# Kernel optimization log

Measured on AMD Instinct MI355X. Metric: run time of the kernel, lower is better.

The kernel has to match this reference:

```python
import jax, jax.numpy as jnp
import numpy as np

B, D, S, K = 4096, 256, 32, 32
TEMP = 1.0

def _unit(x):
    return x / jnp.linalg.norm(x, axis=-1, keepdims=True)

def setup_inputs() -> dict:
    key = jax.random.key(0)
    k1, k2, k3, k4 = jax.random.split(key, 4)
    return {
        "embeddings": _unit(jax.random.normal(k1, (B, D), dtype=jnp.float32)),
        "similar_malicious_embeddings": _unit(jax.random.normal(k2, (B, S, D), dtype=jnp.float32)),
        "diverse_malicious_embeddings": _unit(jax.random.normal(k3, (B, K, D), dtype=jnp.float32)),
        "labels": jax.random.randint(k4, (B,), 0, 2, dtype=jnp.int64),
    }

def reference(embeddings, similar_malicious_embeddings, diverse_malicious_embeddings, labels):
    b = embeddings.shape[0]
    # all pairwise sims zi . zj / T  -> [B, B]
    sims = jnp.matmul(embeddings, embeddings.T) / TEMP
    # sims of zi vs its own similar/diverse sets -> [B, S], [B, K]
    sim_s = jnp.einsum('bd,bsd->bs', embeddings, similar_malicious_embeddings) / TEMP
    sim_d = jnp.einsum('bd,bkd->bk', embeddings, diverse_malicious_embeddings) / TEMP
    not_self = ~jnp.eye(b, dtype=bool)
    # denominator over c_xi = (all embeddings except i) + similar_i + diverse_i
    denom = (jnp.exp(sims) * not_self).sum(-1) + jnp.exp(sim_s).sum(-1) + jnp.exp(sim_d).sum(-1)
    mal = labels == 1
    # d_xi = malicious others (b1_xi) + similar_i + diverse_i
    b1_mask = mal[None, :] & not_self  # [B, B]
    sum_num = (sims * b1_mask).sum(-1) + sim_s.sum(-1) + sim_d.sum(-1)
    cnt = b1_mask.sum(-1) + sim_s.shape[1] + sim_d.shape[1]  # |d_xi| per i (>0 since S,K>0)
    # per zp: -log(exp(s_zp)/denom); averaged over d_xi
    per_i = -sum_num / cnt.astype(sims.dtype) + jnp.log(denom)
    loss = jnp.where(mal, per_i, 0.0).sum() / b
    return loss
```

## Files before the change

kernel.cpp:

```cpp
#include <hip/hip_runtime.h>
#include <stdint.h>

#define BTOT 4096
#define DD   256
#define SS   32
#define KKN  32

typedef unsigned short u16;
using f32x4  = __attribute__((ext_vector_type(4))) float;
using bf16x8 = __attribute__((ext_vector_type(8))) short;

__device__ __forceinline__ u16 f2bf(float f) {
    uint32_t u = __builtin_bit_cast(uint32_t, f);
    u = (u + 0x7FFFu + ((u >> 16) & 1u)) >> 16;
    return (u16)u;
}
__device__ __forceinline__ float bf2f(u16 h) {
    uint32_t u = ((uint32_t)h) << 16;
    return __builtin_bit_cast(float, u);
}

__global__ __launch_bounds__(256) void cast_kernel(const float* __restrict__ E,
                                                   u16* __restrict__ ebf) {
    int idx = blockIdx.x * 256 + threadIdx.x;
    const float4* p = reinterpret_cast<const float4*>(E) + (size_t)idx * 2;
    float4 a = p[0], b = p[1];
    uint4 o;
    o.x = (uint32_t)f2bf(a.x) | ((uint32_t)f2bf(a.y) << 16);
    o.y = (uint32_t)f2bf(a.z) | ((uint32_t)f2bf(a.w) << 16);
    o.z = (uint32_t)f2bf(b.x) | ((uint32_t)f2bf(b.y) << 16);
    o.w = (uint32_t)f2bf(b.z) | ((uint32_t)f2bf(b.w) << 16);
    reinterpret_cast<uint4*>(ebf)[idx] = o;
}

__global__ __launch_bounds__(256) void gemm_kernel(
    const u16* __restrict__ ebf, const int* __restrict__ labels,
    float* __restrict__ gden, float* __restrict__ gnum)
{
    __shared__ u16 As[128 * 32];
    __shared__ u16 Bs[128 * 32];
    __shared__ float rbuf[2][2][128];
    __shared__ float cbuf[2][2][128];

    int bid = blockIdx.x;
    int R = (int)((65.0f - sqrtf(4225.0f - 8.0f * (float)bid)) * 0.5f);
    while (R > 0 && R * (65 - R) / 2 > bid) --R;
    while ((R + 1) * (64 - R) / 2 <= bid) ++R;
    int C = R + (bid - R * (65 - R) / 2);

    int brow = R * 128, bcol = C * 128;
    int t = threadIdx.x, w = t >> 6, lane = t & 63;
    int wr = w >> 1, wc = w & 1;
    int r16 = lane & 15, hi = lane >> 4;
    int kq = hi * 8;

    f32x4 acc[4][4] = {};

    for (int kt = 0; kt < DD / 32; ++kt) {
        int k0 = kt * 32;
        #pragma unroll
        for (int it = 0; it < 2; ++it) {
            int c   = t + 256 * it;
            int row = c >> 2;
            int col = (c & 3) * 8;
            const u16* ga = &ebf[(size_t)(brow + row) * DD + k0 + col];
            const u16* gb = &ebf[(size_t)(bcol + row) * DD + k0 + col];
            __builtin_amdgcn_global_load_lds(
                (const __attribute__((address_space(1))) unsigned int*)ga,
                (__attribute__((address_space(3))) unsigned int*)&As[c * 8], 16, 0, 0);
            __builtin_amdgcn_global_load_lds(
                (const __attribute__((address_space(1))) unsigned int*)gb,
                (__attribute__((address_space(3))) unsigned int*)&Bs[c * 8], 16, 0, 0);
        }
        __syncthreads();

        bf16x8 af[4], bfr[4];
        #pragma unroll
        for (int m = 0; m < 4; ++m)
            af[m] = *(const bf16x8*)&As[(wr * 64 + m * 16 + r16) * 32 + kq];
        #pragma unroll
        for (int n = 0; n < 4; ++n)
            bfr[n] = *(const bf16x8*)&Bs[(wc * 64 + n * 16 + r16) * 32 + kq];
        #pragma unroll
        for (int m = 0; m < 4; ++m)
            #pragma unroll
            for (int n = 0; n < 4; ++n)
                acc[m][n] = __builtin_amdgcn_mfma_f32_16x16x32_bf16(af[m], bfr[n], acc[m][n], 0, 0, 0);
        __syncthreads();
    }

    bool offdiag = (C != R);

    float malf[4];
    #pragma unroll
    for (int n = 0; n < 4; ++n)
        malf[n] = (float)labels[bcol + wc * 64 + n * 16 + r16];
    float malr[16];
    #pragma unroll
    for (int m = 0; m < 4; ++m)
        #pragma unroll
        for (int r = 0; r < 4; ++r)
            malr[m * 4 + r] = (float)labels[brow + wr * 64 + m * 16 + hi * 4 + r];

    float cd[4] = {0.f, 0.f, 0.f, 0.f}, cn[4] = {0.f, 0.f, 0.f, 0.f};

    #pragma unroll
    for (int m = 0; m < 4; ++m) {
        #pragma unroll
        for (int r = 0; r < 4; ++r) {
            float pe = 0.f, pn = 0.f;
            #pragma unroll
            for (int n = 0; n < 4; ++n) {
                float v  = acc[m][n][r];
                float ex = __expf(v);
                pe += ex;
                pn += malf[n] * v;
                cd[n] += ex;
                cn[n] += malr[m * 4 + r] * v;
            }
            #pragma unroll
            for (int s = 1; s < 16; s <<= 1) {
                pe += __shfl_xor(pe, s, 64);
                pn += __shfl_xor(pn, s, 64);
            }
            if (r16 == 0) {
                int rl = wr * 64 + m * 16 + hi * 4 + r;
                rbuf[0][wc][rl] = pe;
                rbuf[1][wc][rl] = pn;
            }
        }
    }

    if (offdiag) {
        #pragma unroll
        for (int n = 0; n < 4; ++n) {
            cd[n] += __shfl_xor(cd[n], 16, 64);
            cd[n] += __shfl_xor(cd[n], 32, 64);
            cn[n] += __shfl_xor(cn[n], 16, 64);
            cn[n] += __shfl_xor(cn[n], 32, 64);
            if (lane < 16) {
                int cl = wc * 64 + n * 16 + lane;
                cbuf[0][wr][cl] = cd[n];
                cbuf[1][wr][cl] = cn[n];
            }
        }
    }
    __syncthreads();

    if (t < 128) {
        int i = brow + t;
        gden[(size_t)i * 32 + C] = rbuf[0][0][t] + rbuf[0][1][t];
        gnum[(size_t)i * 32 + C] = rbuf[1][0][t] + rbuf[1][1][t];
    } else if (offdiag) {
        int tt = t - 128;
        int j = bcol + tt;
        gden[(size_t)j * 32 + R] = cbuf[0][0][tt] + cbuf[0][1][tt];
        gnum[(size_t)j * 32 + R] = cbuf[1][0][tt] + cbuf[1][1][tt];
    }
}

__global__ __launch_bounds__(256) void simdiv_kernel(
    const float* __restrict__ E, const float* __restrict__ Sim, const float* __restrict__ Div,
    const int* __restrict__ labels, float* __restrict__ sdden, float* __restrict__ sdnum)
{
    extern __shared__ float lds[];
    int i = blockIdx.x;
    int t = threadIdx.x, w = t >> 6, lane = t & 63;
    int g = lane >> 4, sub = lane & 15;

    const float4* E4 = reinterpret_cast<const float4*>(E + (size_t)i * DD);
    float4 e0 = E4[0 * 16 + sub], e1 = E4[1 * 16 + sub];
    float4 e2 = E4[2 * 16 + sub], e3 = E4[3 * 16 + sub];

    #pragma unroll
    for (int vt = 0; vt < 16; ++vt) {
        int v = w * 16 + vt;
        const float* src = (v < SS) ? (Sim + ((size_t)i * SS + v) * DD)
                                    : (Div + ((size_t)i * KKN + (v - SS)) * DD);
        __builtin_amdgcn_global_load_lds(
            (const __attribute__((address_space(1))) unsigned int*)(src + lane * 4),
            (__attribute__((address_space(3))) unsigned int*)(lds + (size_t)v * DD), 16, 0, 0);
    }

    float accs = 0.f, acce = 0.f;

#define SD_STEP(VT, CNT)                                                          \
    {                                                                             \
        asm volatile("s_waitcnt vmcnt(" #CNT ")" ::: "memory");                   \
        int v = w * 16 + (VT) * 4 + g;                                            \
        const float4* row = reinterpret_cast<const float4*>(lds + (size_t)v * DD);\
        float4 s0 = row[0 * 16 + sub], s1 = row[1 * 16 + sub];                    \
        float4 s2 = row[2 * 16 + sub], s3 = row[3 * 16 + sub];                    \
        float d = e0.x * s0.x + e0.y * s0.y + e0.z * s0.z + e0.w * s0.w           \
                + e1.x * s1.x + e1.y * s1.y + e1.z * s1.z + e1.w * s1.w           \
                + e2.x * s2.x + e2.y * s2.y + e2.z * s2.z + e2.w * s2.w           \
                + e3.x * s3.x + e3.y * s3.y + e3.z * s3.z + e3.w * s3.w;          \
        d += __shfl_xor(d, 1, 64);                                                \
        d += __shfl_xor(d, 2, 64);                                                \
        d += __shfl_xor(d, 4, 64);                                                \
        d += __shfl_xor(d, 8, 64);                                                \
        accs += d;                                                                \
        acce += __expf(d);                                                        \
    }

    SD_STEP(0, 12)
    SD_STEP(1, 8)
    SD_STEP(2, 4)
    SD_STEP(3, 0)
#undef SD_STEP

    accs += __shfl_xor(accs, 16, 64);
    accs += __shfl_xor(accs, 32, 64);
    acce += __shfl_xor(acce, 16, 64);
    acce += __shfl_xor(acce, 32, 64);

    float sd = 0.f;
    {
        float c;
        c = bf2f(f2bf(e0.x)); sd += c * c;  c = bf2f(f2bf(e0.y)); sd += c * c;
        c = bf2f(f2bf(e0.z)); sd += c * c;  c = bf2f(f2bf(e0.w)); sd += c * c;
        c = bf2f(f2bf(e1.x)); sd += c * c;  c = bf2f(f2bf(e1.y)); sd += c * c;
        c = bf2f(f2bf(e1.z)); sd += c * c;  c = bf2f(f2bf(e1.w)); sd += c * c;
        c = bf2f(f2bf(e2.x)); sd += c * c;  c = bf2f(f2bf(e2.y)); sd += c * c;
        c = bf2f(f2bf(e2.z)); sd += c * c;  c = bf2f(f2bf(e2.w)); sd += c * c;
        c = bf2f(f2bf(e3.x)); sd += c * c;  c = bf2f(f2bf(e3.y)); sd += c * c;
        c = bf2f(f2bf(e3.z)); sd += c * c;  c = bf2f(f2bf(e3.w)); sd += c * c;
    }
    sd += __shfl_xor(sd, 1, 64);
    sd += __shfl_xor(sd, 2, 64);
    sd += __shfl_xor(sd, 4, 64);
    sd += __shfl_xor(sd, 8, 64);

    if (lane == 0) {
        float addn = accs, addd = acce;
        if (w == 0) {
            addd -= __expf(sd);
            addn -= (float)labels[i] * sd;
        }
        atomicAdd(&sdnum[i], addn);
        atomicAdd(&sdden[i], addd);
    }
}

__global__ __launch_bounds__(128) void reduce1_kernel(
    const int* __restrict__ labels, const float* __restrict__ gden,
    const float* __restrict__ gnum, const float* __restrict__ sdden,
    const float* __restrict__ sdnum, float* __restrict__ part)
{
    __shared__ float sA[128], sB[128];
    __shared__ int   sC[128];
    int p = blockIdx.x, t = threadIdx.x;
    int i = p * 128 + t;

    const float4* dr = reinterpret_cast<const float4*>(gden + (size_t)i * 32);
    const float4* nr = reinterpret_cast<const float4*>(gnum + (size_t)i * 32);
    float den = sdden[i], num = sdnum[i];
    #pragma unroll
    for (int c = 0; c < 8; ++c) {
        float4 a = dr[c]; den += a.x + a.y + a.z + a.w;
        float4 b = nr[c]; num += b.x + b.y + b.z + b.w;
    }
    int lab = labels[i];
    sA[t] = lab ? __logf(den) : 0.f;
    sB[t] = lab ? num : 0.f;
    sC[t] = lab;
    __syncthreads();
    for (int s = 64; s > 0; s >>= 1) {
        if (t < s) { sA[t] += sA[t + s]; sB[t] += sB[t + s]; sC[t] += sC[t + s]; }
        __syncthreads();
    }
    if (t == 0) {
        part[p]      = sA[0];
        part[32 + p] = sB[0];
        part[64 + p] = (float)sC[0];
    }
}

__global__ __launch_bounds__(64) void final_kernel(const float* __restrict__ part,
                                                   float* __restrict__ out)
{
    int lane = threadIdx.x;
    float lg = (lane < 32) ? part[lane]      : 0.f;
    float nm = (lane < 32) ? part[32 + lane] : 0.f;
    float ml = (lane < 32) ? part[64 + lane] : 0.f;
    #pragma unroll
    for (int s = 1; s < 64; s <<= 1) {
        lg += __shfl_xor(lg, s, 64);
        nm += __shfl_xor(nm, s, 64);
        ml += __shfl_xor(ml, s, 64);
    }
    if (lane == 0) {
        float cnt = ml - 1.f + (float)(SS + KKN);
        out[0] = (lg - nm / cnt) / (float)BTOT;
    }
}

extern "C" void kernel_launch(void* const* d_in, const int* in_sizes, int n_in,
                              void* d_out, int out_size, void* d_ws, size_t ws_size,
                              hipStream_t stream) {
    const float* E   = (const float*)d_in[0];
    const float* Sim = (const float*)d_in[1];
    const float* Div = (const float*)d_in[2];
    const int* labels = (const int*)d_in[3];
    float* out = (float*)d_out;

    char* ws = (char*)d_ws;
    u16*   ebf   = (u16*)ws;                              ws += (size_t)BTOT * DD * sizeof(u16);
    float* gden  = (float*)ws;                            ws += (size_t)BTOT * 32 * sizeof(float);
    float* gnum  = (float*)ws;                            ws += (size_t)BTOT * 32 * sizeof(float);
    float* sdden = (float*)ws;                            ws += BTOT * sizeof(float);
    float* sdnum = (float*)ws;                            ws += BTOT * sizeof(float);
    float* part  = (float*)ws;

    hipMemsetAsync(sdden, 0, 2 * BTOT * sizeof(float), stream);
    cast_kernel<<<BTOT * DD / 8 / 256, 256, 0, stream>>>(E, ebf);
    gemm_kernel<<<528, 256, 0, stream>>>(ebf, labels, gden, gnum);
    simdiv_kernel<<<BTOT, 256, 64 * 1024, stream>>>(E, Sim, Div, labels, sdden, sdnum);
    reduce1_kernel<<<32, 128, 0, stream>>>(labels, gden, gnum, sdden, sdnum, part);
    final_kernel<<<1, 64, 0, stream>>>(part, out);
}
```

Before: 78.55 us.

## Merge GEMM and sim/div kernels into one interleaved launch, drop memset and atomics

```diff
diff --git a/kernel.cpp b/kernel.cpp
--- a/kernel.cpp
+++ b/kernel.cpp
@@ -5,6 +5,8 @@
 #define DD   256
 #define SS   32
 #define KKN  32
+#define NGEMM 528
+#define NBLK  (BTOT + NGEMM)
 
 typedef unsigned short u16;
 using f32x4  = __attribute__((ext_vector_type(4))) float;
@@ -33,156 +35,163 @@
     reinterpret_cast<uint4*>(ebf)[idx] = o;
 }
 
-__global__ __launch_bounds__(256) void gemm_kernel(
+__global__ __launch_bounds__(256) void fat_kernel(
+    const float* __restrict__ E, const float* __restrict__ Sim, const float* __restrict__ Div,
     const u16* __restrict__ ebf, const int* __restrict__ labels,
-    float* __restrict__ gden, float* __restrict__ gnum)
+    float* __restrict__ gden, float* __restrict__ gnum,
+    float* __restrict__ sdden, float* __restrict__ sdnum)
 {
-    __shared__ u16 As[128 * 32];
-    __shared__ u16 Bs[128 * 32];
-    __shared__ float rbuf[2][2][128];
-    __shared__ float cbuf[2][2][128];
-
-    int bid = blockIdx.x;
-    int R = (int)((65.0f - sqrtf(4225.0f - 8.0f * (float)bid)) * 0.5f);
-    while (R > 0 && R * (65 - R) / 2 > bid) --R;
-    while ((R + 1) * (64 - R) / 2 <= bid) ++R;
-    int C = R + (bid - R * (65 - R) / 2);
-
-    int brow = R * 128, bcol = C * 128;
-    int t = threadIdx.x, w = t >> 6, lane = t & 63;
-    int wr = w >> 1, wc = w & 1;
-    int r16 = lane & 15, hi = lane >> 4;
-    int kq = hi * 8;
-
-    f32x4 acc[4][4] = {};
-
-    for (int kt = 0; kt < DD / 32; ++kt) {
-        int k0 = kt * 32;
+    extern __shared__ char dyn[];
+    int bid  = blockIdx.x;
+    int t    = threadIdx.x;
+    int w    = t >> 6;
+    int lane = t & 63;
+
+    bool is_gemm = (bid < NGEMM * 8) && ((bid & 7) == 7);
+
+    if (is_gemm) {
+        u16*   As   = (u16*)dyn;
+        u16*   Bs   = (u16*)(dyn + 8192);
+        float* rbuf = (float*)(dyn + 16384);
+        float* cbuf = (float*)(dyn + 16384 + 2048);
+
+        int g = bid >> 3;
+        int R = (int)((65.0f - sqrtf(4225.0f - 8.0f * (float)g)) * 0.5f);
+        while (R > 0 && R * (65 - R) / 2 > g) --R;
+        while ((R + 1) * (64 - R) / 2 <= g) ++R;
+        int C = R + (g - R * (65 - R) / 2);
+
+        int brow = R * 128, bcol = C * 128;
+        int wr = w >> 1, wc = w & 1;
+        int r16 = lane & 15, hi = lane >> 4;
+        int kq = hi * 8;
+
+        f32x4 acc[4][4] = {};
+
+        for (int kt = 0; kt < DD / 32; ++kt) {
+            int k0 = kt * 32;
+            #pragma unroll
+            for (int it = 0; it < 2; ++it) {
+                int c   = t + 256 * it;
+                int row = c >> 2;
+                int col = (c & 3) * 8;
+                const u16* ga = &ebf[(size_t)(brow + row) * DD + k0 + col];
+                const u16* gb = &ebf[(size_t)(bcol + row) * DD + k0 + col];
+                __builtin_amdgcn_global_load_lds(
+                    (const __attribute__((address_space(1))) unsigned int*)ga,
+                    (__attribute__((address_space(3))) unsigned int*)&As[c * 8], 16, 0, 0);
+                __builtin_amdgcn_global_load_lds(
+                    (const __attribute__((address_space(1))) unsigned int*)gb,
+                    (__attribute__((address_space(3))) unsigned int*)&Bs[c * 8], 16, 0, 0);
+            }
+            __syncthreads();
+
+            bf16x8 af[4], bfr[4];
+            #pragma unroll
+            for (int m = 0; m < 4; ++m)
+                af[m] = *(const bf16x8*)&As[(wr * 64 + m * 16 + r16) * 32 + kq];
+            #pragma unroll
+            for (int n = 0; n < 4; ++n)
+                bfr[n] = *(const bf16x8*)&Bs[(wc * 64 + n * 16 + r16) * 32 + kq];
+            #pragma unroll
+            for (int m = 0; m < 4; ++m)
+                #pragma unroll
+                for (int n = 0; n < 4; ++n)
+                    acc[m][n] = __builtin_amdgcn_mfma_f32_16x16x32_bf16(af[m], bfr[n], acc[m][n], 0, 0, 0);
+            __syncthreads();
+        }
+
+        bool offdiag = (C != R);
+
+        float malf[4];
         #pragma unroll
-        for (int it = 0; it < 2; ++it) {
-            int c   = t + 256 * it;
-            int row = c >> 2;
-            int col = (c & 3) * 8;
-            const u16* ga = &ebf[(size_t)(brow + row) * DD + k0 + col];
-            const u16* gb = &ebf[(size_t)(bcol + row) * DD + k0 + col];
-            __builtin_amdgcn_global_load_lds(
-                (const __attribute__((address_space(1))) unsigned int*)ga,
-                (__attribute__((address_space(3))) unsigned int*)&As[c * 8], 16, 0, 0);
-            __builtin_amdgcn_global_load_lds(
-                (const __attribute__((address_space(1))) unsigned int*)gb,
-                (__attribute__((address_space(3))) unsigned int*)&Bs[c * 8], 16, 0, 0);
-        }
-        __syncthreads();
-
-        bf16x8 af[4], bfr[4];
+        for (int n = 0; n < 4; ++n)
+            malf[n] = (float)labels[bcol + wc * 64 + n * 16 + r16];
+        float malr[16];
         #pragma unroll
         for (int m = 0; m < 4; ++m)
-            af[m] = *(const bf16x8*)&As[(wr * 64 + m * 16 + r16) * 32 + kq];
+            #pragma unroll
+            for (int r = 0; r < 4; ++r)
+                malr[m * 4 + r] = (float)labels[brow + wr * 64 + m * 16 + hi * 4 + r];
+
+        float cd[4] = {0.f, 0.f, 0.f, 0.f}, cn[4] = {0.f, 0.f, 0.f, 0.f};
+
         #pragma unroll
-        for (int n = 0; n < 4; ++n)
-            bfr[n] = *(const bf16x8*)&Bs[(wc * 64 + n * 16 + r16) * 32 + kq];
+        for (int m = 0; m < 4; ++m) {
+            #pragma unroll
+            for (int r = 0; r < 4; ++r) {
+                float pe = 0.f, pn = 0.f;
+                #pragma unroll
+                for (int n = 0; n < 4; ++n) {
+                    float v  = acc[m][n][r];
+                    float ex = __expf(v);
+                    pe += ex;
+                    pn += malf[n] * v;
+                    cd[n] += ex;
+                    cn[n] += malr[m * 4 + r] * v;
+                }
+                #pragma unroll
+                for (int s = 1; s < 16; s <<= 1) {
+                    pe += __shfl_xor(pe, s, 64);
+                    pn += __shfl_xor(pn, s, 64);
+                }
+                if (r16 == 0) {
+                    int rl = wr * 64 + m * 16 + hi * 4 + r;
+                    rbuf[0 * 256 + wc * 128 + rl] = pe;
+                    rbuf[1 * 256 + wc * 128 + rl] = pn;
+                }
+            }
+        }
+
+        if (offdiag) {
+            #pragma unroll
+            for (int n = 0; n < 4; ++n) {
+                cd[n] += __shfl_xor(cd[n], 16, 64);
+                cd[n] += __shfl_xor(cd[n], 32, 64);
+                cn[n] += __shfl_xor(cn[n], 16, 64);
+                cn[n] += __shfl_xor(cn[n], 32, 64);
+                if (lane < 16) {
+                    int cl = wc * 64 + n * 16 + lane;
+                    cbuf[0 * 256 + wr * 128 + cl] = cd[n];
+                    cbuf[1 * 256 + wr * 128 + cl] = cn[n];
+                }
+            }
+        }
+        __syncthreads();
+
+        if (t < 128) {
+            int i = brow + t;
+            gden[(size_t)i * 32 + C] = rbuf[0 * 256 + 0 + t] + rbuf[0 * 256 + 128 + t];
+            gnum[(size_t)i * 32 + C] = rbuf[1 * 256 + 0 + t] + rbuf[1 * 256 + 128 + t];
+        } else if (offdiag) {
+            int tt = t - 128;
+            int j = bcol + tt;
+            gden[(size_t)j * 32 + R] = cbuf[0 * 256 + 0 + tt] + cbuf[0 * 256 + 128 + tt];
+            gnum[(size_t)j * 32 + R] = cbuf[1 * 256 + 0 + tt] + cbuf[1 * 256 + 128 + tt];
+        }
+    } else {
+        float* lds  = (float*)dyn;
+        float* sbuf = (float*)(dyn + 64 * 1024);
+
+        int i = (bid < NGEMM * 8) ? bid - (bid >> 3) : bid - NGEMM;
+        int g = lane >> 4, sub = lane & 15;
+
+        const float4* E4 = reinterpret_cast<const float4*>(E + (size_t)i * DD);
+        float4 e0 = E4[0 * 16 + sub], e1 = E4[1 * 16 + sub];
+        float4 e2 = E4[2 * 16 + sub], e3 = E4[3 * 16 + sub];
+        asm volatile("" ::: "memory");
+
         #pragma unroll
-        for (int m = 0; m < 4; ++m)
-            #pragma unroll
-            for (int n = 0; n < 4; ++n)
-                acc[m][n] = __builtin_amdgcn_mfma_f32_16x16x32_bf16(af[m], bfr[n], acc[m][n], 0, 0, 0);
-        __syncthreads();
-    }
-
-    bool offdiag = (C != R);
-
-    float malf[4];
-    #pragma unroll
-    for (int n = 0; n < 4; ++n)
-        malf[n] = (float)labels[bcol + wc * 64 + n * 16 + r16];
-    float malr[16];
-    #pragma unroll
-    for (int m = 0; m < 4; ++m)
-        #pragma unroll
-        for (int r = 0; r < 4; ++r)
-            malr[m * 4 + r] = (float)labels[brow + wr * 64 + m * 16 + hi * 4 + r];
-
-    float cd[4] = {0.f, 0.f, 0.f, 0.f}, cn[4] = {0.f, 0.f, 0.f, 0.f};
-
-    #pragma unroll
-    for (int m = 0; m < 4; ++m) {
-        #pragma unroll
-        for (int r = 0; r < 4; ++r) {
-            float pe = 0.f, pn = 0.f;
-            #pragma unroll
-            for (int n = 0; n < 4; ++n) {
-                float v  = acc[m][n][r];
-                float ex = __expf(v);
-                pe += ex;
-                pn += malf[n] * v;
-                cd[n] += ex;
-                cn[n] += malr[m * 4 + r] * v;
-            }
-            #pragma unroll
-            for (int s = 1; s < 16; s <<= 1) {
-                pe += __shfl_xor(pe, s, 64);
-                pn += __shfl_xor(pn, s, 64);
-            }
-            if (r16 == 0) {
-                int rl = wr * 64 + m * 16 + hi * 4 + r;
-                rbuf[0][wc][rl] = pe;
-                rbuf[1][wc][rl] = pn;
-            }
-        }
-    }
-
-    if (offdiag) {
-        #pragma unroll
-        for (int n = 0; n < 4; ++n) {
-            cd[n] += __shfl_xor(cd[n], 16, 64);
-            cd[n] += __shfl_xor(cd[n], 32, 64);
-            cn[n] += __shfl_xor(cn[n], 16, 64);
-            cn[n] += __shfl_xor(cn[n], 32, 64);
-            if (lane < 16) {
-                int cl = wc * 64 + n * 16 + lane;
-                cbuf[0][wr][cl] = cd[n];
-                cbuf[1][wr][cl] = cn[n];
-            }
-        }
-    }
-    __syncthreads();
-
-    if (t < 128) {
-        int i = brow + t;
-        gden[(size_t)i * 32 + C] = rbuf[0][0][t] + rbuf[0][1][t];
-        gnum[(size_t)i * 32 + C] = rbuf[1][0][t] + rbuf[1][1][t];
-    } else if (offdiag) {
-        int tt = t - 128;
-        int j = bcol + tt;
-        gden[(size_t)j * 32 + R] = cbuf[0][0][tt] + cbuf[0][1][tt];
-        gnum[(size_t)j * 32 + R] = cbuf[1][0][tt] + cbuf[1][1][tt];
-    }
-}
-
-__global__ __launch_bounds__(256) void simdiv_kernel(
-    const float* __restrict__ E, const float* __restrict__ Sim, const float* __restrict__ Div,
-    const int* __restrict__ labels, float* __restrict__ sdden, float* __restrict__ sdnum)
-{
-    extern __shared__ float lds[];
-    int i = blockIdx.x;
-    int t = threadIdx.x, w = t >> 6, lane = t & 63;
-    int g = lane >> 4, sub = lane & 15;
-
-    const float4* E4 = reinterpret_cast<const float4*>(E + (size_t)i * DD);
-    float4 e0 = E4[0 * 16 + sub], e1 = E4[1 * 16 + sub];
-    float4 e2 = E4[2 * 16 + sub], e3 = E4[3 * 16 + sub];
-
-    #pragma unroll
-    for (int vt = 0; vt < 16; ++vt) {
-        int v = w * 16 + vt;
-        const float* src = (v < SS) ? (Sim + ((size_t)i * SS + v) * DD)
-                                    : (Div + ((size_t)i * KKN + (v - SS)) * DD);
-        __builtin_amdgcn_global_load_lds(
-            (const __attribute__((address_space(1))) unsigned int*)(src + lane * 4),
-            (__attribute__((address_space(3))) unsigned int*)(lds + (size_t)v * DD), 16, 0, 0);
-    }
-
-    float accs = 0.f, acce = 0.f;
+        for (int vt = 0; vt < 16; ++vt) {
+            int v = w * 16 + vt;
+            const float* src = (v < SS) ? (Sim + ((size_t)i * SS + v) * DD)
+                                        : (Div + ((size_t)i * KKN + (v - SS)) * DD);
+            __builtin_amdgcn_global_load_lds(
+                (const __attribute__((address_space(1))) unsigned int*)(src + lane * 4),
+                (__attribute__((address_space(3))) unsigned int*)(lds + (size_t)v * DD), 16, 0, 0);
+        }
+
+        float accs = 0.f, acce = 0.f;
 
 #define SD_STEP(VT, CNT)                                                          \
     {                                                                             \
@@ -203,42 +212,49 @@
         acce += __expf(d);                                                        \
     }
 
-    SD_STEP(0, 12)
-    SD_STEP(1, 8)
-    SD_STEP(2, 4)
-    SD_STEP(3, 0)
+        SD_STEP(0, 12)
+        SD_STEP(1, 8)
+        SD_STEP(2, 4)
+        SD_STEP(3, 0)
 #undef SD_STEP
 
-    accs += __shfl_xor(accs, 16, 64);
-    accs += __shfl_xor(accs, 32, 64);
-    acce += __shfl_xor(acce, 16, 64);
-    acce += __shfl_xor(acce, 32, 64);
-
-    float sd = 0.f;
-    {
-        float c;
-        c = bf2f(f2bf(e0.x)); sd += c * c;  c = bf2f(f2bf(e0.y)); sd += c * c;
-        c = bf2f(f2bf(e0.z)); sd += c * c;  c = bf2f(f2bf(e0.w)); sd += c * c;
-        c = bf2f(f2bf(e1.x)); sd += c * c;  c = bf2f(f2bf(e1.y)); sd += c * c;
-        c = bf2f(f2bf(e1.z)); sd += c * c;  c = bf2f(f2bf(e1.w)); sd += c * c;
-        c = bf2f(f2bf(e2.x)); sd += c * c;  c = bf2f(f2bf(e2.y)); sd += c * c;
-        c = bf2f(f2bf(e2.z)); sd += c * c;  c = bf2f(f2bf(e2.w)); sd += c * c;
-        c = bf2f(f2bf(e3.x)); sd += c * c;  c = bf2f(f2bf(e3.y)); sd += c * c;
-        c = bf2f(f2bf(e3.z)); sd += c * c;  c = bf2f(f2bf(e3.w)); sd += c * c;
-    }
-    sd += __shfl_xor(sd, 1, 64);
-    sd += __shfl_xor(sd, 2, 64);
-    sd += __shfl_xor(sd, 4, 64);
-    sd += __shfl_xor(sd, 8, 64);
-
-    if (lane == 0) {
-        float addn = accs, addd = acce;
+        accs += __shfl_xor(accs, 16, 64);
+        accs += __shfl_xor(accs, 32, 64);
+        acce += __shfl_xor(acce, 16, 64);
+        acce += __shfl_xor(acce, 32, 64);
+
+        float sd = 0.f;
         if (w == 0) {
-            addd -= __expf(sd);
-            addn -= (float)labels[i] * sd;
-        }
-        atomicAdd(&sdnum[i], addn);
-        atomicAdd(&sdden[i], addd);
+            float c;
+            c = bf2f(f2bf(e0.x)); sd += c * c;  c = bf2f(f2bf(e0.y)); sd += c * c;
+            c = bf2f(f2bf(e0.z)); sd += c * c;  c = bf2f(f2bf(e0.w)); sd += c * c;
+            c = bf2f(f2bf(e1.x)); sd += c * c;  c = bf2f(f2bf(e1.y)); sd += c * c;
+            c = bf2f(f2bf(e1.z)); sd += c * c;  c = bf2f(f2bf(e1.w)); sd += c * c;
+            c = bf2f(f2bf(e2.x)); sd += c * c;  c = bf2f(f2bf(e2.y)); sd += c * c;
+            c = bf2f(f2bf(e2.z)); sd += c * c;  c = bf2f(f2bf(e2.w)); sd += c * c;
+            c = bf2f(f2bf(e3.x)); sd += c * c;  c = bf2f(f2bf(e3.y)); sd += c * c;
+            c = bf2f(f2bf(e3.z)); sd += c * c;  c = bf2f(f2bf(e3.w)); sd += c * c;
+            sd += __shfl_xor(sd, 1, 64);
+            sd += __shfl_xor(sd, 2, 64);
+            sd += __shfl_xor(sd, 4, 64);
+            sd += __shfl_xor(sd, 8, 64);
+        }
+
+        __syncthreads();
+        if (lane == 0) {
+            float addn = accs, addd = acce;
+            if (w == 0) {
+                addd -= __expf(sd);
+                addn -= (float)labels[i] * sd;
+            }
+            sbuf[w * 2]     = addn;
+            sbuf[w * 2 + 1] = addd;
+        }
+        __syncthreads();
+        if (t == 0) {
+            sdnum[i] = sbuf[0] + sbuf[2] + sbuf[4] + sbuf[6];
+            sdden[i] = sbuf[1] + sbuf[3] + sbuf[5] + sbuf[7];
+        }
     }
 }
 
@@ -305,17 +321,16 @@
     float* out = (float*)d_out;
 
     char* ws = (char*)d_ws;
-    u16*   ebf   = (u16*)ws;                              ws += (size_t)BTOT * DD * sizeof(u16);
-    float* gden  = (float*)ws;                            ws += (size_t)BTOT * 32 * sizeof(float);
-    float* gnum  = (float*)ws;                            ws += (size_t)BTOT * 32 * sizeof(float);
-    float* sdden = (float*)ws;                            ws += BTOT * sizeof(float);
-    float* sdnum = (float*)ws;                            ws += BTOT * sizeof(float);
+    u16*   ebf   = (u16*)ws;   ws += (size_t)BTOT * DD * sizeof(u16);
+    float* gden  = (float*)ws; ws += (size_t)BTOT * 32 * sizeof(float);
+    float* gnum  = (float*)ws; ws += (size_t)BTOT * 32 * sizeof(float);
+    float* sdden = (float*)ws; ws += BTOT * sizeof(float);
+    float* sdnum = (float*)ws; ws += BTOT * sizeof(float);
     float* part  = (float*)ws;
 
-    hipMemsetAsync(sdden, 0, 2 * BTOT * sizeof(float), stream);
     cast_kernel<<<BTOT * DD / 8 / 256, 256, 0, stream>>>(E, ebf);
-    gemm_kernel<<<528, 256, 0, stream>>>(ebf, labels, gden, gnum);
-    simdiv_kernel<<<BTOT, 256, 64 * 1024, stream>>>(E, Sim, Div, labels, sdden, sdnum);
+    fat_kernel<<<NBLK, 256, 64 * 1024 + 64, stream>>>(E, Sim, Div, ebf, labels,
+                                                      gden, gnum, sdden, sdnum);
     reduce1_kernel<<<32, 128, 0, stream>>>(labels, gden, gnum, sdden, sdnum, part);
     final_kernel<<<1, 64, 0, stream>>>(part, out);
 }
```

Result: slower. 105.0 us (+33.7%).

## Pipeline simdiv over 8 rows per block and drop atomics and memset

Applied to the files above, without the earlier changes.

```diff
diff --git a/kernel.cpp b/kernel.cpp
--- a/kernel.cpp
+++ b/kernel.cpp
@@ -5,6 +5,9 @@
 #define DD   256
 #define SS   32
 #define KKN  32
+#define NGEMM 528
+#define NROWB 8
+#define SDBLK (BTOT / NROWB)
 
 typedef unsigned short u16;
 using f32x4  = __attribute__((ext_vector_type(4))) float;
@@ -161,91 +164,134 @@
 
 __global__ __launch_bounds__(256) void simdiv_kernel(
     const float* __restrict__ E, const float* __restrict__ Sim, const float* __restrict__ Div,
-    const int* __restrict__ labels, float* __restrict__ sdden, float* __restrict__ sdnum)
+    float* __restrict__ sdpart)
 {
-    extern __shared__ float lds[];
-    int i = blockIdx.x;
+    extern __shared__ char dyn[];
+    float* stg = (float*)dyn;
+    float* eld = (float*)(dyn + 65536);
+    float* scr = (float*)(dyn + 65536 + 8192);
+
+    int b = blockIdx.x;
     int t = threadIdx.x, w = t >> 6, lane = t & 63;
     int g = lane >> 4, sub = lane & 15;
-
-    const float4* E4 = reinterpret_cast<const float4*>(E + (size_t)i * DD);
-    float4 e0 = E4[0 * 16 + sub], e1 = E4[1 * 16 + sub];
-    float4 e2 = E4[2 * 16 + sub], e3 = E4[3 * 16 + sub];
-
-    #pragma unroll
-    for (int vt = 0; vt < 16; ++vt) {
-        int v = w * 16 + vt;
-        const float* src = (v < SS) ? (Sim + ((size_t)i * SS + v) * DD)
-                                    : (Div + ((size_t)i * KKN + (v - SS)) * DD);
-        __builtin_amdgcn_global_load_lds(
-            (const __attribute__((address_space(1))) unsigned int*)(src + lane * 4),
-            (__attribute__((address_space(3))) unsigned int*)(lds + (size_t)v * DD), 16, 0, 0);
-    }
-
-    float accs = 0.f, acce = 0.f;
-
-#define SD_STEP(VT, CNT)                                                          \
-    {                                                                             \
-        asm volatile("s_waitcnt vmcnt(" #CNT ")" ::: "memory");                   \
-        int v = w * 16 + (VT) * 4 + g;                                            \
-        const float4* row = reinterpret_cast<const float4*>(lds + (size_t)v * DD);\
-        float4 s0 = row[0 * 16 + sub], s1 = row[1 * 16 + sub];                    \
-        float4 s2 = row[2 * 16 + sub], s3 = row[3 * 16 + sub];                    \
-        float d = e0.x * s0.x + e0.y * s0.y + e0.z * s0.z + e0.w * s0.w           \
-                + e1.x * s1.x + e1.y * s1.y + e1.z * s1.z + e1.w * s1.w           \
-                + e2.x * s2.x + e2.y * s2.y + e2.z * s2.z + e2.w * s2.w           \
-                + e3.x * s3.x + e3.y * s3.y + e3.z * s3.z + e3.w * s3.w;          \
-        d += __shfl_xor(d, 1, 64);                                                \
-        d += __shfl_xor(d, 2, 64);                                                \
-        d += __shfl_xor(d, 4, 64);                                                \
-        d += __shfl_xor(d, 8, 64);                                                \
-        accs += d;                                                                \
-        acce += __expf(d);                                                        \
-    }
-
-    SD_STEP(0, 12)
-    SD_STEP(1, 8)
-    SD_STEP(2, 4)
-    SD_STEP(3, 0)
-#undef SD_STEP
-
-    accs += __shfl_xor(accs, 16, 64);
-    accs += __shfl_xor(accs, 32, 64);
-    acce += __shfl_xor(acce, 16, 64);
-    acce += __shfl_xor(acce, 32, 64);
-
-    float sd = 0.f;
-    {
-        float c;
-        c = bf2f(f2bf(e0.x)); sd += c * c;  c = bf2f(f2bf(e0.y)); sd += c * c;
-        c = bf2f(f2bf(e0.z)); sd += c * c;  c = bf2f(f2bf(e0.w)); sd += c * c;
-        c = bf2f(f2bf(e1.x)); sd += c * c;  c = bf2f(f2bf(e1.y)); sd += c * c;
-        c = bf2f(f2bf(e1.z)); sd += c * c;  c = bf2f(f2bf(e1.w)); sd += c * c;
-        c = bf2f(f2bf(e2.x)); sd += c * c;  c = bf2f(f2bf(e2.y)); sd += c * c;
-        c = bf2f(f2bf(e2.z)); sd += c * c;  c = bf2f(f2bf(e2.w)); sd += c * c;
-        c = bf2f(f2bf(e3.x)); sd += c * c;  c = bf2f(f2bf(e3.y)); sd += c * c;
-        c = bf2f(f2bf(e3.z)); sd += c * c;  c = bf2f(f2bf(e3.w)); sd += c * c;
-    }
-    sd += __shfl_xor(sd, 1, 64);
-    sd += __shfl_xor(sd, 2, 64);
-    sd += __shfl_xor(sd, 4, 64);
-    sd += __shfl_xor(sd, 8, 64);
-
-    if (lane == 0) {
-        float addn = accs, addd = acce;
-        if (w == 0) {
-            addd -= __expf(sd);
-            addn -= (float)labels[i] * sd;
-        }
-        atomicAdd(&sdnum[i], addn);
-        atomicAdd(&sdden[i], addd);
-    }
+    int i0 = b * NROWB;
+
+    float* wstg = stg + w * 16 * 256;
+    float* weld = eld + w * 2 * 256;
+
+#define STAGE_E(I, P)                                                                        \
+    __builtin_amdgcn_global_load_lds(                                                        \
+        (const __attribute__((address_space(1))) unsigned int*)(E + (size_t)(I) * DD + lane * 4), \
+        (__attribute__((address_space(3))) unsigned int*)(weld + (P) * 256), 16, 0, 0)
+
+#define STAGE_V(I, Q)                                                                        \
+    {                                                                                        \
+        int v_ = w * 16 + (Q);                                                               \
+        const float* s_ = (v_ < SS) ? (Sim + ((size_t)(I) * SS + v_) * DD)                   \
+                                    : (Div + ((size_t)(I) * KKN + (v_ - SS)) * DD);          \
+        __builtin_amdgcn_global_load_lds(                                                    \
+            (const __attribute__((address_space(1))) unsigned int*)(s_ + lane * 4),          \
+            (__attribute__((address_space(3))) unsigned int*)(wstg + (Q) * 256), 16, 0, 0);  \
+    }
+
+#define COMP(CC)                                                                             \
+    {                                                                                        \
+        const float4* row_ = (const float4*)(wstg + ((CC) * 4 + g) * 256);                   \
+        float4 s0 = row_[0 * 16 + sub], s1 = row_[1 * 16 + sub];                             \
+        float4 s2 = row_[2 * 16 + sub], s3 = row_[3 * 16 + sub];                             \
+        float d = e0.x * s0.x + e0.y * s0.y + e0.z * s0.z + e0.w * s0.w                      \
+                + e1.x * s1.x + e1.y * s1.y + e1.z * s1.z + e1.w * s1.w                      \
+                + e2.x * s2.x + e2.y * s2.y + e2.z * s2.z + e2.w * s2.w                      \
+                + e3.x * s3.x + e3.y * s3.y + e3.z * s3.z + e3.w * s3.w;                     \
+        d += __shfl_xor(d, 1, 64);                                                           \
+        d += __shfl_xor(d, 2, 64);                                                           \
+        d += __shfl_xor(d, 4, 64);                                                           \
+        d += __shfl_xor(d, 8, 64);                                                           \
+        accs += d;                                                                           \
+        acce += __expf(d);                                                                   \
+    }
+
+    STAGE_E(i0, 0);
+    #pragma unroll
+    for (int q = 0; q < 16; ++q) STAGE_V(i0, q);
+
+    #pragma unroll 1
+    for (int r = 0; r < NROWB; ++r) {
+        int i = i0 + r;
+        int p = r & 1;
+        bool more = (r < NROWB - 1);
+
+        float accs = 0.f, acce = 0.f;
+        float4 e0, e1, e2, e3;
+
+        asm volatile("s_waitcnt vmcnt(12)" ::: "memory");
+        {
+            const float4* ep = (const float4*)(weld + p * 256);
+            e0 = ep[0 * 16 + sub]; e1 = ep[1 * 16 + sub];
+            e2 = ep[2 * 16 + sub]; e3 = ep[3 * 16 + sub];
+        }
+        COMP(0)
+        if (more) {
+            STAGE_E(i + 1, p ^ 1);
+            STAGE_V(i + 1, 0) STAGE_V(i + 1, 1) STAGE_V(i + 1, 2) STAGE_V(i + 1, 3)
+        }
+
+        if (more) { asm volatile("s_waitcnt vmcnt(13)" ::: "memory"); }
+        else      { asm volatile("s_waitcnt vmcnt(8)"  ::: "memory"); }
+        COMP(1)
+        if (more) { STAGE_V(i + 1, 4) STAGE_V(i + 1, 5) STAGE_V(i + 1, 6) STAGE_V(i + 1, 7) }
+
+        if (more) { asm volatile("s_waitcnt vmcnt(13)" ::: "memory"); }
+        else      { asm volatile("s_waitcnt vmcnt(4)"  ::: "memory"); }
+        COMP(2)
+        if (more) { STAGE_V(i + 1, 8) STAGE_V(i + 1, 9) STAGE_V(i + 1, 10) STAGE_V(i + 1, 11) }
+
+        if (more) { asm volatile("s_waitcnt vmcnt(13)" ::: "memory"); }
+        else      { asm volatile("s_waitcnt vmcnt(0)"  ::: "memory"); }
+        COMP(3)
+        if (more) { STAGE_V(i + 1, 12) STAGE_V(i + 1, 13) STAGE_V(i + 1, 14) STAGE_V(i + 1, 15) }
+
+        accs += __shfl_xor(accs, 16, 64);
+        accs += __shfl_xor(accs, 32, 64);
+        acce += __shfl_xor(acce, 16, 64);
+        acce += __shfl_xor(acce, 32, 64);
+
+        float sd = 0.f;
+        {
+            float c;
+            c = bf2f(f2bf(e0.x)); sd += c * c;  c = bf2f(f2bf(e0.y)); sd += c * c;
+            c = bf2f(f2bf(e0.z)); sd += c * c;  c = bf2f(f2bf(e0.w)); sd += c * c;
+            c = bf2f(f2bf(e1.x)); sd += c * c;  c = bf2f(f2bf(e1.y)); sd += c * c;
+            c = bf2f(f2bf(e1.z)); sd += c * c;  c = bf2f(f2bf(e1.w)); sd += c * c;
+            c = bf2f(f2bf(e2.x)); sd += c * c;  c = bf2f(f2bf(e2.y)); sd += c * c;
+            c = bf2f(f2bf(e2.z)); sd += c * c;  c = bf2f(f2bf(e2.w)); sd += c * c;
+            c = bf2f(f2bf(e3.x)); sd += c * c;  c = bf2f(f2bf(e3.y)); sd += c * c;
+            c = bf2f(f2bf(e3.z)); sd += c * c;  c = bf2f(f2bf(e3.w)); sd += c * c;
+        }
+        sd += __shfl_xor(sd, 1, 64);
+        sd += __shfl_xor(sd, 2, 64);
+        sd += __shfl_xor(sd, 4, 64);
+        sd += __shfl_xor(sd, 8, 64);
+
+        if (lane == 0) {
+            scr[r * 12 + w * 2]     = accs;
+            scr[r * 12 + w * 2 + 1] = acce;
+        }
+        if (t == 0) scr[r * 12 + 8] = sd;
+    }
+
+    __syncthreads();
+    if (t < NROWB * 12) sdpart[(size_t)b * (NROWB * 12) + t] = scr[t];
+
+#undef STAGE_E
+#undef STAGE_V
+#undef COMP
 }
 
 __global__ __launch_bounds__(128) void reduce1_kernel(
     const int* __restrict__ labels, const float* __restrict__ gden,
-    const float* __restrict__ gnum, const float* __restrict__ sdden,
-    const float* __restrict__ sdnum, float* __restrict__ part)
+    const float* __restrict__ gnum, const float* __restrict__ sdpart,
+    float* __restrict__ part)
 {
     __shared__ float sA[128], sB[128];
     __shared__ int   sC[128];
@@ -254,13 +300,20 @@
 
     const float4* dr = reinterpret_cast<const float4*>(gden + (size_t)i * 32);
     const float4* nr = reinterpret_cast<const float4*>(gnum + (size_t)i * 32);
-    float den = sdden[i], num = sdnum[i];
+    const float* sp = sdpart + (size_t)(i >> 3) * (NROWB * 12) + (i & 7) * 12;
+
+    float num = sp[0] + sp[2] + sp[4] + sp[6];
+    float den = sp[1] + sp[3] + sp[5] + sp[7];
+    float sdv = sp[8];
+    int lab = labels[i];
+    den -= __expf(sdv);
+    num -= lab ? sdv : 0.f;
+
     #pragma unroll
     for (int c = 0; c < 8; ++c) {
         float4 a = dr[c]; den += a.x + a.y + a.z + a.w;
         float4 b = nr[c]; num += b.x + b.y + b.z + b.w;
     }
-    int lab = labels[i];
     sA[t] = lab ? __logf(den) : 0.f;
     sB[t] = lab ? num : 0.f;
     sC[t] = lab;
@@ -305,17 +358,15 @@
     float* out = (float*)d_out;
 
     char* ws = (char*)d_ws;
-    u16*   ebf   = (u16*)ws;                              ws += (size_t)BTOT * DD * sizeof(u16);
-    float* gden  = (float*)ws;                            ws += (size_t)BTOT * 32 * sizeof(float);
-    float* gnum  = (float*)ws;                            ws += (size_t)BTOT * 32 * sizeof(float);
-    float* sdden = (float*)ws;                            ws += BTOT * sizeof(float);
-    float* sdnum = (float*)ws;                            ws += BTOT * sizeof(float);
-    float* part  = (float*)ws;
-
-    hipMemsetAsync(sdden, 0, 2 * BTOT * sizeof(float), stream);
+    u16*   ebf    = (u16*)ws;   ws += (size_t)BTOT * DD * sizeof(u16);
+    float* gden   = (float*)ws; ws += (size_t)BTOT * 32 * sizeof(float);
+    float* gnum   = (float*)ws; ws += (size_t)BTOT * 32 * sizeof(float);
+    float* sdpart = (float*)ws; ws += (size_t)SDBLK * NROWB * 12 * sizeof(float);
+    float* part   = (float*)ws;
+
     cast_kernel<<<BTOT * DD / 8 / 256, 256, 0, stream>>>(E, ebf);
-    gemm_kernel<<<528, 256, 0, stream>>>(ebf, labels, gden, gnum);
-    simdiv_kernel<<<BTOT, 256, 64 * 1024, stream>>>(E, Sim, Div, labels, sdden, sdnum);
-    reduce1_kernel<<<32, 128, 0, stream>>>(labels, gden, gnum, sdden, sdnum, part);
+    gemm_kernel<<<NGEMM, 256, 0, stream>>>(ebf, labels, gden, gnum);
+    simdiv_kernel<<<SDBLK, 256, 65536 + 8192 + 384, stream>>>(E, Sim, Div, sdpart);
+    reduce1_kernel<<<32, 128, 0, stream>>>(labels, gden, gnum, sdpart, part);
     final_kernel<<<1, 64, 0, stream>>>(part, out);
 }
```

New measurement: 77.69 us. Within noise of the previous version (-1.1%).

## Restructure simdiv to one wave per row with register-pipelined loads

Applied to the files above, without the earlier changes.

```diff
diff --git a/kernel.cpp b/kernel.cpp
--- a/kernel.cpp
+++ b/kernel.cpp
@@ -5,6 +5,7 @@
 #define DD   256
 #define SS   32
 #define KKN  32
+#define NGEMM 528
 
 typedef unsigned short u16;
 using f32x4  = __attribute__((ext_vector_type(4))) float;
@@ -159,55 +160,70 @@
     }
 }
 
-__global__ __launch_bounds__(256) void simdiv_kernel(
+__global__ __launch_bounds__(256, 4) void simdiv_kernel(
     const float* __restrict__ E, const float* __restrict__ Sim, const float* __restrict__ Div,
-    const int* __restrict__ labels, float* __restrict__ sdden, float* __restrict__ sdnum)
+    float* __restrict__ sdpart)
 {
-    extern __shared__ float lds[];
-    int i = blockIdx.x;
-    int t = threadIdx.x, w = t >> 6, lane = t & 63;
+    int i    = blockIdx.x * 4 + (threadIdx.x >> 6);
+    int lane = threadIdx.x & 63;
     int g = lane >> 4, sub = lane & 15;
 
-    const float4* E4 = reinterpret_cast<const float4*>(E + (size_t)i * DD);
-    float4 e0 = E4[0 * 16 + sub], e1 = E4[1 * 16 + sub];
-    float4 e2 = E4[2 * 16 + sub], e3 = E4[3 * 16 + sub];
-
-    #pragma unroll
-    for (int vt = 0; vt < 16; ++vt) {
-        int v = w * 16 + vt;
-        const float* src = (v < SS) ? (Sim + ((size_t)i * SS + v) * DD)
-                                    : (Div + ((size_t)i * KKN + (v - SS)) * DD);
-        __builtin_amdgcn_global_load_lds(
-            (const __attribute__((address_space(1))) unsigned int*)(src + lane * 4),
-            (__attribute__((address_space(3))) unsigned int*)(lds + (size_t)v * DD), 16, 0, 0);
-    }
-
+    const char* Eb = (const char*)(E + (size_t)i * DD);
+    float4 e0 = *(const float4*)(Eb + 0 * 256 + sub * 16);
+    float4 e1 = *(const float4*)(Eb + 1 * 256 + sub * 16);
+    float4 e2 = *(const float4*)(Eb + 2 * 256 + sub * 16);
+    float4 e3 = *(const float4*)(Eb + 3 * 256 + sub * 16);
+
+    const char* Sb = (const char*)(Sim + (size_t)i * SS * DD) + g * 1024 + sub * 16;
+    const char* Db = (const char*)(Div + (size_t)i * KKN * DD) + g * 1024 + sub * 16;
+
+    float4 buf[4][4];
     float accs = 0.f, acce = 0.f;
 
-#define SD_STEP(VT, CNT)                                                          \
-    {                                                                             \
-        asm volatile("s_waitcnt vmcnt(" #CNT ")" ::: "memory");                   \
-        int v = w * 16 + (VT) * 4 + g;                                            \
-        const float4* row = reinterpret_cast<const float4*>(lds + (size_t)v * DD);\
-        float4 s0 = row[0 * 16 + sub], s1 = row[1 * 16 + sub];                    \
-        float4 s2 = row[2 * 16 + sub], s3 = row[3 * 16 + sub];                    \
-        float d = e0.x * s0.x + e0.y * s0.y + e0.z * s0.z + e0.w * s0.w           \
-                + e1.x * s1.x + e1.y * s1.y + e1.z * s1.z + e1.w * s1.w           \
-                + e2.x * s2.x + e2.y * s2.y + e2.z * s2.z + e2.w * s2.w           \
-                + e3.x * s3.x + e3.y * s3.y + e3.z * s3.z + e3.w * s3.w;          \
-        d += __shfl_xor(d, 1, 64);                                                \
-        d += __shfl_xor(d, 2, 64);                                                \
-        d += __shfl_xor(d, 4, 64);                                                \
-        d += __shfl_xor(d, 8, 64);                                                \
-        accs += d;                                                                \
-        acce += __expf(d);                                                        \
-    }
-
-    SD_STEP(0, 12)
-    SD_STEP(1, 8)
-    SD_STEP(2, 4)
-    SD_STEP(3, 0)
-#undef SD_STEP
+#define ISSUE(SET)                                                                  \
+    {                                                                               \
+        const char* b_ = ((SET) < 8) ? (Sb + (SET) * 4096) : (Db + ((SET) - 8) * 4096); \
+        buf[(SET) & 3][0] = *(const float4*)(b_ + 0);                               \
+        buf[(SET) & 3][1] = *(const float4*)(b_ + 256);                             \
+        buf[(SET) & 3][2] = *(const float4*)(b_ + 512);                             \
+        buf[(SET) & 3][3] = *(const float4*)(b_ + 768);                             \
+    }
+
+#define COMPUTE(SET)                                                                \
+    {                                                                               \
+        float4 s0 = buf[(SET) & 3][0], s1 = buf[(SET) & 3][1];                      \
+        float4 s2 = buf[(SET) & 3][2], s3 = buf[(SET) & 3][3];                      \
+        float d = e0.x * s0.x + e0.y * s0.y + e0.z * s0.z + e0.w * s0.w             \
+                + e1.x * s1.x + e1.y * s1.y + e1.z * s1.z + e1.w * s1.w             \
+                + e2.x * s2.x + e2.y * s2.y + e2.z * s2.z + e2.w * s2.w             \
+                + e3.x * s3.x + e3.y * s3.y + e3.z * s3.z + e3.w * s3.w;            \
+        d += __shfl_xor(d, 1, 64);                                                  \
+        d += __shfl_xor(d, 2, 64);                                                  \
+        d += __shfl_xor(d, 4, 64);                                                  \
+        d += __shfl_xor(d, 8, 64);                                                  \
+        accs += d;                                                                  \
+        acce += __expf(d);                                                          \
+    }
+
+    ISSUE(0) ISSUE(1) ISSUE(2) ISSUE(3)
+    COMPUTE(0)  ISSUE(4)
+    COMPUTE(1)  ISSUE(5)
+    COMPUTE(2)  ISSUE(6)
+    COMPUTE(3)  ISSUE(7)
+    COMPUTE(4)  ISSUE(8)
+    COMPUTE(5)  ISSUE(9)
+    COMPUTE(6)  ISSUE(10)
+    COMPUTE(7)  ISSUE(11)
+    COMPUTE(8)  ISSUE(12)
+    COMPUTE(9)  ISSUE(13)
+    COMPUTE(10) ISSUE(14)
+    COMPUTE(11) ISSUE(15)
+    COMPUTE(12)
+    COMPUTE(13)
+    COMPUTE(14)
+    COMPUTE(15)
+#undef ISSUE
+#undef COMPUTE
 
     accs += __shfl_xor(accs, 16, 64);
     accs += __shfl_xor(accs, 32, 64);
@@ -232,20 +248,15 @@
     sd += __shfl_xor(sd, 8, 64);
 
     if (lane == 0) {
-        float addn = accs, addd = acce;
-        if (w == 0) {
-            addd -= __expf(sd);
-            addn -= (float)labels[i] * sd;
-        }
-        atomicAdd(&sdnum[i], addn);
-        atomicAdd(&sdden[i], addd);
+        float4 o; o.x = accs; o.y = acce; o.z = sd; o.w = 0.f;
+        *(float4*)(sdpart + (size_t)i * 4) = o;
     }
 }
 
 __global__ __launch_bounds__(128) void reduce1_kernel(
     const int* __restrict__ labels, const float* __restrict__ gden,
-    const float* __restrict__ gnum, const float* __restrict__ sdden,
-    const float* __restrict__ sdnum, float* __restrict__ part)
+    const float* __restrict__ gnum, const float* __restrict__ sdpart,
+    float* __restrict__ part)
 {
     __shared__ float sA[128], sB[128];
     __shared__ int   sC[128];
@@ -254,13 +265,20 @@
 
     const float4* dr = reinterpret_cast<const float4*>(gden + (size_t)i * 32);
     const float4* nr = reinterpret_cast<const float4*>(gnum + (size_t)i * 32);
-    float den = sdden[i], num = sdnum[i];
+    float4 sp = *(const float4*)(sdpart + (size_t)i * 4);
+
+    float num = sp.x;
+    float den = sp.y;
+    float sdv = sp.z;
+    int lab = labels[i];
+    den -= __expf(sdv);
+    num -= lab ? sdv : 0.f;
+
     #pragma unroll
     for (int c = 0; c < 8; ++c) {
         float4 a = dr[c]; den += a.x + a.y + a.z + a.w;
         float4 b = nr[c]; num += b.x + b.y + b.z + b.w;
     }
-    int lab = labels[i];
     sA[t] = lab ? __logf(den) : 0.f;
     sB[t] = lab ? num : 0.f;
     sC[t] = lab;
@@ -305,17 +323,15 @@
     float* out = (float*)d_out;
 
     char* ws = (char*)d_ws;
-    u16*   ebf   = (u16*)ws;                              ws += (size_t)BTOT * DD * sizeof(u16);
-    float* gden  = (float*)ws;                            ws += (size_t)BTOT * 32 * sizeof(float);
-    float* gnum  = (float*)ws;                            ws += (size_t)BTOT * 32 * sizeof(float);
-    float* sdden = (float*)ws;                            ws += BTOT * sizeof(float);
-    float* sdnum = (float*)ws;                            ws += BTOT * sizeof(float);
-    float* part  = (float*)ws;
-
-    hipMemsetAsync(sdden, 0, 2 * BTOT * sizeof(float), stream);
+    u16*   ebf    = (u16*)ws;   ws += (size_t)BTOT * DD * sizeof(u16);
+    float* gden   = (float*)ws; ws += (size_t)BTOT * 32 * sizeof(float);
+    float* gnum   = (float*)ws; ws += (size_t)BTOT * 32 * sizeof(float);
+    float* sdpart = (float*)ws; ws += (size_t)BTOT * 4 * sizeof(float);
+    float* part   = (float*)ws;
+
     cast_kernel<<<BTOT * DD / 8 / 256, 256, 0, stream>>>(E, ebf);
-    gemm_kernel<<<528, 256, 0, stream>>>(ebf, labels, gden, gnum);
-    simdiv_kernel<<<BTOT, 256, 64 * 1024, stream>>>(E, Sim, Div, labels, sdden, sdnum);
-    reduce1_kernel<<<32, 128, 0, stream>>>(labels, gden, gnum, sdden, sdnum, part);
+    gemm_kernel<<<NGEMM, 256, 0, stream>>>(ebf, labels, gden, gnum);
+    simdiv_kernel<<<BTOT / 4, 256, 0, stream>>>(E, Sim, Div, sdpart);
+    reduce1_kernel<<<32, 128, 0, stream>>>(labels, gden, gnum, sdpart, part);
     final_kernel<<<1, 64, 0, stream>>>(part, out);
 }
```

Result: faster. 76.10 us (-3.1%).
